# Kernel optimization log

Hardware: AMD Instinct MI355X
Metric: run time of the kernel (lower is better)

The kernel has to match this reference:

```python
import jax, jax.numpy as jnp
import numpy as np

N = 100000
E = 1600000
H = 64      # hidden_size
NH = 8      # num_heads
DH = H // NH  # per-head dim (heads are the LAST axis, as in the torch code)


def _lin(x, W, b):
    return x @ W + b


def setup_inputs() -> dict:
    key = jax.random.key(0)
    ks = jax.random.split(key, 18)
    s = 0.05
    inp = {
        "h_x": jax.random.normal(ks[0], (N, H), jnp.float32),
        "h_e": jax.random.normal(ks[1], (E, H), jnp.float32),
        "row": jax.random.randint(ks[2], (E,), 0, N, jnp.int32),  # dst node of each nonzero
        "col": jax.random.randint(ks[3], (E,), 0, N, jnp.int32),  # src node of each nonzero
    }
    names = ["q", "k", "v", "e", "oh", "oe"]
    for i, nm in enumerate(names):
        inp["W" + nm] = jax.random.normal(ks[4 + 2 * i], (H, H), jnp.float32) * s
        inp["b" + nm] = jax.random.normal(ks[5 + 2 * i], (H,), jnp.float32) * s
    return inp


def reference(h_x, h_e, row, col, Wq, bq, Wk, bk, Wv, bv, We, be, Woh, boh, Woe, boe):
    n = h_x.shape[0]
    m = h_e.shape[0]
    q = _lin(h_x, Wq, bq).reshape(n, DH, NH)
    k = _lin(h_x, Wk, bk).reshape(n, DH, NH)
    v = _lin(h_x, Wv, bv).reshape(n, DH, NH)
    e = _lin(h_e, We, be).reshape(m, DH, NH)

    # SDDMM: per-nonzero (i=row, j=col), per-head dot of q[i] and k[j]  -> (E, NH)
    scores = (q[row] * k[col]).sum(axis=1) / jnp.sqrt(jnp.float32(DH))

    # edge gating: e.sum over dh axis -> (E, NH)
    e_gate = e.sum(axis=1)
    scores = scores * e_gate

    # oe branch (uses pre-softmax gated scores)
    oe_feat = scores[:, None, :] * e          # (E, DH, NH)
    oe = _lin(oe_feat.reshape(m, H), Woe, boe)

    # sparse softmax over dim=1 (per destination row), per head
    mx = jax.ops.segment_max(scores, row, num_segments=n)      # (N, NH)
    ex = jnp.exp(scores - mx[row])
    den = jax.ops.segment_sum(ex, row, num_segments=n)         # (N, NH)
    sm = ex / den[row]                                          # (E, NH)

    # bSpMM: h_out[i,:,h] = sum_{e: row[e]=i} sm[e,h] * v[col[e],:,h]
    h_out = jax.ops.segment_sum(sm[:, None, :] * v[col], row, num_segments=n)
    oh = _lin(h_out.reshape(n, H), Woh, boh)
    return (oh, oe)
```

## Files before the change

kernel.cpp:

```cpp
#include <hip/hip_runtime.h>

typedef __attribute__((ext_vector_type(8))) short bf16x8;
typedef __attribute__((ext_vector_type(4))) float f32x4;

__device__ __forceinline__ unsigned short f2bf(float f) {
  unsigned u = __float_as_uint(f);
  return (unsigned short)((u + 0x7fffu + ((u >> 16) & 1u)) >> 16);
}
__device__ __forceinline__ float bf2f(unsigned short h) {
  return __uint_as_float(((unsigned)h) << 16);
}

__device__ __forceinline__ void lds_fence() {
  asm volatile("s_waitcnt lgkmcnt(0)" ::: "memory");
  __builtin_amdgcn_sched_barrier(0);
}

template<bool IN_BF16, bool OUT_BF16>
__global__ void __launch_bounds__(256) gemm64_kernel(const void* __restrict__ Ain,
    const float* __restrict__ W, const float* __restrict__ bias,
    void* __restrict__ Out, int M) {
  const int tid = threadIdx.x;
  const int l = tid & 63;
  const int g = l >> 4;
  const int n15 = l & 15;

  bf16x8 bfrag[4][2];
  float bv[4];
#pragma unroll
  for (int nb = 0; nb < 4; ++nb) {
    bv[nb] = bias[nb * 16 + n15];
#pragma unroll
    for (int kb = 0; kb < 2; ++kb)
#pragma unroll
      for (int j = 0; j < 8; ++j)
        bfrag[nb][kb][j] = (short)f2bf(W[(kb * 32 + g * 8 + j) * 64 + nb * 16 + n15]);
  }

  int wid = (blockIdx.x * blockDim.x + tid) >> 6;
  int nw = (gridDim.x * blockDim.x) >> 6;
  int ntiles = (M + 15) >> 4;
  for (int t = wid; t < ntiles; t += nw) {
    int m0 = t << 4;
    int arow = m0 + n15;
    bf16x8 a0, a1;
    if (arow < M) {
      if constexpr (IN_BF16) {
        const unsigned short* ap = (const unsigned short*)Ain + (size_t)arow * 64 + g * 8;
        a0 = *(const bf16x8*)ap;
        a1 = *(const bf16x8*)(ap + 32);
      } else {
        const float* ap = (const float*)Ain + (size_t)arow * 64 + g * 8;
        f32x4 x0 = *(const f32x4*)ap, x1 = *(const f32x4*)(ap + 4);
        f32x4 x2 = *(const f32x4*)(ap + 32), x3 = *(const f32x4*)(ap + 36);
#pragma unroll
        for (int j = 0; j < 4; ++j) {
          a0[j] = (short)f2bf(x0[j]); a0[4 + j] = (short)f2bf(x1[j]);
          a1[j] = (short)f2bf(x2[j]); a1[4 + j] = (short)f2bf(x3[j]);
        }
      }
    } else {
#pragma unroll
      for (int j = 0; j < 8; ++j) { a0[j] = 0; a1[j] = 0; }
    }
    f32x4 acc[4];
#pragma unroll
    for (int nb = 0; nb < 4; ++nb) {
      acc[nb] = (f32x4){bv[nb], bv[nb], bv[nb], bv[nb]};
      acc[nb] = __builtin_amdgcn_mfma_f32_16x16x32_bf16(a0, bfrag[nb][0], acc[nb], 0, 0, 0);
      acc[nb] = __builtin_amdgcn_mfma_f32_16x16x32_bf16(a1, bfrag[nb][1], acc[nb], 0, 0, 0);
    }
#pragma unroll
    for (int nb = 0; nb < 4; ++nb)
#pragma unroll
      for (int r = 0; r < 4; ++r) {
        int orow = m0 + g * 4 + r;
        if (orow < M) {
          float val = acc[nb][r];
          size_t oidx = (size_t)orow * 64 + nb * 16 + n15;
          if constexpr (OUT_BF16) ((unsigned short*)Out)[oidx] = f2bf(val);
          else                    ((float*)Out)[oidx] = val;
        }
      }
  }
}

__global__ void __launch_bounds__(256) qkv3_kernel(const float* __restrict__ hx,
    const float* __restrict__ Wq, const float* __restrict__ bq,
    const float* __restrict__ Wk, const float* __restrict__ bk,
    const float* __restrict__ Wv, const float* __restrict__ bv,
    unsigned short* __restrict__ q, unsigned short* __restrict__ k,
    unsigned short* __restrict__ v, int M) {
  const int tid = threadIdx.x;
  const int l = tid & 63;
  const int g = l >> 4;
  const int n15 = l & 15;
  const float* Ws[3] = {Wq, Wk, Wv};
  const float* bs[3] = {bq, bk, bv};
  unsigned short* outs[3] = {q, k, v};

  bf16x8 bfrag[3][4][2];
  float bvv[3][4];
#pragma unroll
  for (int w = 0; w < 3; ++w)
#pragma unroll
    for (int nb = 0; nb < 4; ++nb) {
      bvv[w][nb] = bs[w][nb * 16 + n15];
#pragma unroll
      for (int kb = 0; kb < 2; ++kb)
#pragma unroll
        for (int j = 0; j < 8; ++j)
          bfrag[w][nb][kb][j] = (short)f2bf(Ws[w][(kb * 32 + g * 8 + j) * 64 + nb * 16 + n15]);
    }

  int wid = (blockIdx.x * blockDim.x + tid) >> 6;
  int nw = (gridDim.x * blockDim.x) >> 6;
  int ntiles = (M + 15) >> 4;
  for (int t = wid; t < ntiles; t += nw) {
    int m0 = t << 4;
    int arow = m0 + n15;
    bf16x8 a0, a1;
    if (arow < M) {
      const float* ap = hx + (size_t)arow * 64 + g * 8;
      f32x4 x0 = *(const f32x4*)ap, x1 = *(const f32x4*)(ap + 4);
      f32x4 x2 = *(const f32x4*)(ap + 32), x3 = *(const f32x4*)(ap + 36);
#pragma unroll
      for (int j = 0; j < 4; ++j) {
        a0[j] = (short)f2bf(x0[j]); a0[4 + j] = (short)f2bf(x1[j]);
        a1[j] = (short)f2bf(x2[j]); a1[4 + j] = (short)f2bf(x3[j]);
      }
    } else {
#pragma unroll
      for (int j = 0; j < 8; ++j) { a0[j] = 0; a1[j] = 0; }
    }
#pragma unroll
    for (int w = 0; w < 3; ++w) {
      f32x4 acc[4];
#pragma unroll
      for (int nb = 0; nb < 4; ++nb) {
        acc[nb] = (f32x4){bvv[w][nb], bvv[w][nb], bvv[w][nb], bvv[w][nb]};
        acc[nb] = __builtin_amdgcn_mfma_f32_16x16x32_bf16(a0, bfrag[w][nb][0], acc[nb], 0, 0, 0);
        acc[nb] = __builtin_amdgcn_mfma_f32_16x16x32_bf16(a1, bfrag[w][nb][1], acc[nb], 0, 0, 0);
      }
#pragma unroll
      for (int nb = 0; nb < 4; ++nb)
#pragma unroll
        for (int r = 0; r < 4; ++r) {
          int orow = m0 + g * 4 + r;
          if (orow < M)
            outs[w][(size_t)orow * 64 + nb * 16 + n15] = f2bf(acc[nb][r]);
        }
    }
  }
}

__global__ void __launch_bounds__(256) edge_fused_kernel(
    const float* __restrict__ he,
    const int* __restrict__ rowi, const int* __restrict__ coli,
    const int* __restrict__ eslot,
    const unsigned short* __restrict__ qb, const unsigned short* __restrict__ kbuf,
    const float* __restrict__ We, const float* __restrict__ be,
    const float* __restrict__ Woe, const float* __restrict__ boe,
    float* __restrict__ oe, float* __restrict__ escores, int E) {
  const int tid = threadIdx.x;
  const int wv = tid >> 6;
  const int l = tid & 63;
  const int g = l >> 4;
  const int n15 = l & 15;
  const int h = n15 & 7;

  __shared__ float s_lds[4][160];
  __shared__ unsigned short feat_lds[4][16 * 72];

  bf16x8 bfE[4][2], bfO[4][2];
  float beV[4], boV[4];
#pragma unroll
  for (int nb = 0; nb < 4; ++nb) {
    beV[nb] = be[nb * 16 + n15];
    boV[nb] = boe[nb * 16 + n15];
#pragma unroll
    for (int kb = 0; kb < 2; ++kb)
#pragma unroll
      for (int j = 0; j < 8; ++j) {
        bfE[nb][kb][j] = (short)f2bf(We[(kb * 32 + g * 8 + j) * 64 + nb * 16 + n15]);
        bfO[nb][kb][j] = (short)f2bf(Woe[(kb * 32 + g * 8 + j) * 64 + nb * 16 + n15]);
      }
  }

  const int ntiles = (E + 15) >> 4;
  const int nit = (ntiles + 3) >> 2;
  for (int it = blockIdx.x; it < nit; it += gridDim.x) {
    const int m0 = ((it << 2) + wv) << 4;
    const int arow = m0 + n15;
    bf16x8 a0, a1;
    if (arow < E) {
      const float* ap = he + (size_t)arow * 64 + g * 8;
      f32x4 x0 = *(const f32x4*)ap, x1 = *(const f32x4*)(ap + 4);
      f32x4 x2 = *(const f32x4*)(ap + 32), x3 = *(const f32x4*)(ap + 36);
#pragma unroll
      for (int j = 0; j < 4; ++j) {
        a0[j] = (short)f2bf(x0[j]); a0[4 + j] = (short)f2bf(x1[j]);
        a1[j] = (short)f2bf(x2[j]); a1[4 + j] = (short)f2bf(x3[j]);
      }
    } else {
#pragma unroll
      for (int j = 0; j < 8; ++j) { a0[j] = 0; a1[j] = 0; }
    }
    f32x4 acc[4];
#pragma unroll
    for (int nb = 0; nb < 4; ++nb) {
      acc[nb] = (f32x4){beV[nb], beV[nb], beV[nb], beV[nb]};
      acc[nb] = __builtin_amdgcn_mfma_f32_16x16x32_bf16(a0, bfE[nb][0], acc[nb], 0, 0, 0);
      acc[nb] = __builtin_amdgcn_mfma_f32_16x16x32_bf16(a1, bfE[nb][1], acc[nb], 0, 0, 0);
    }
    float gc[4];
#pragma unroll
    for (int r = 0; r < 4; ++r) {
      float s = acc[0][r] + acc[1][r] + acc[2][r] + acc[3][r];
      s += __shfl_xor(s, 8, 64);
      gc[r] = s * 0.35355339059327373f;
    }
    const int esafe = (arow < E) ? arow : (E - 1);
    const int rq = rowi[esafe], rc = coli[esafe];
    const int slotv = eslot[esafe];
    const unsigned short* qp = qb + (size_t)rq * 64 + g * 16;
    const unsigned short* kp = kbuf + (size_t)rc * 64 + g * 16;
    bf16x8 qv0 = *(const bf16x8*)qp, qv1 = *(const bf16x8*)(qp + 8);
    bf16x8 kv0 = *(const bf16x8*)kp, kv1 = *(const bf16x8*)(kp + 8);
    float p[8];
#pragma unroll
    for (int j = 0; j < 8; ++j)
      p[j] = bf2f((unsigned short)qv0[j]) * bf2f((unsigned short)kv0[j])
           + bf2f((unsigned short)qv1[j]) * bf2f((unsigned short)kv1[j]);
#pragma unroll
    for (int j = 0; j < 8; ++j) {
      p[j] += __shfl_xor(p[j], 16, 64);
      p[j] += __shfl_xor(p[j], 32, 64);
    }
    if (l < 16) {
      float2* sp = (float2*)&s_lds[wv][n15 * 10];
#pragma unroll
      for (int j = 0; j < 4; ++j) sp[j] = make_float2(p[2 * j], p[2 * j + 1]);
    }
    lds_fence();
    float srow[4];
#pragma unroll
    for (int r = 0; r < 4; ++r)
      srow[r] = s_lds[wv][(g * 4 + r) * 10 + h] * gc[r];
#pragma unroll
    for (int r = 0; r < 4; ++r) {
      int orow = m0 + g * 4 + r;
      int slot = __shfl(slotv, g * 4 + r, 64);
      if (n15 < 8 && orow < E) escores[(size_t)slot * 8 + n15] = srow[r];
    }
#pragma unroll
    for (int nb = 0; nb < 4; ++nb)
#pragma unroll
      for (int r = 0; r < 4; ++r)
        feat_lds[wv][(g * 4 + r) * 72 + nb * 16 + n15] = f2bf(srow[r] * acc[nb][r]);
    lds_fence();
    const unsigned short* fpt = &feat_lds[wv][n15 * 72 + g * 8];
    a0 = *(const bf16x8*)fpt;
    a1 = *(const bf16x8*)(fpt + 32);
#pragma unroll
    for (int nb = 0; nb < 4; ++nb) {
      f32x4 a2 = (f32x4){boV[nb], boV[nb], boV[nb], boV[nb]};
      a2 = __builtin_amdgcn_mfma_f32_16x16x32_bf16(a0, bfO[nb][0], a2, 0, 0, 0);
      a2 = __builtin_amdgcn_mfma_f32_16x16x32_bf16(a1, bfO[nb][1], a2, 0, 0, 0);
#pragma unroll
      for (int r = 0; r < 4; ++r) {
        int orow = m0 + g * 4 + r;
        if (orow < E) oe[(size_t)orow * 64 + nb * 16 + n15] = a2[r];
      }
    }
  }
}

__global__ void zero_kernel(int* __restrict__ p, int n) {
  int i = blockIdx.x * blockDim.x + threadIdx.x;
  if (i < n) p[i] = 0;
}

__global__ void hist_kernel(const int* __restrict__ row, int* __restrict__ deg, int E) {
  int gid = blockIdx.x * blockDim.x + threadIdx.x;
  if (gid < E) atomicAdd(&deg[row[gid]], 1);
}

#define SCAN_B 256
#define SCAN_E 8
__global__ void scan1_kernel(const int* __restrict__ deg, int* __restrict__ rowptr,
                             int* __restrict__ blksum, int n) {
  __shared__ int sh[SCAN_B];
  int base = blockIdx.x * (SCAN_B * SCAN_E) + threadIdx.x * SCAN_E;
  int v[SCAN_E];
  int s = 0;
#pragma unroll
  for (int j = 0; j < SCAN_E; ++j) {
    v[j] = (base + j < n) ? deg[base + j] : 0;
    s += v[j];
  }
  sh[threadIdx.x] = s;
  __syncthreads();
  for (int off = 1; off < SCAN_B; off <<= 1) {
    int t = (threadIdx.x >= off) ? sh[threadIdx.x - off] : 0;
    __syncthreads();
    sh[threadIdx.x] += t;
    __syncthreads();
  }
  if (threadIdx.x == SCAN_B - 1) blksum[blockIdx.x] = sh[SCAN_B - 1];
  int run = sh[threadIdx.x] - s;
#pragma unroll
  for (int j = 0; j < SCAN_E; ++j) {
    if (base + j < n) rowptr[base + j] = run;
    run += v[j];
  }
}

__global__ void scan2_kernel(int* __restrict__ blksum, int nb) {
  __shared__ int sh[SCAN_B];
  int v = (threadIdx.x < nb) ? blksum[threadIdx.x] : 0;
  sh[threadIdx.x] = v;
  __syncthreads();
  for (int off = 1; off < SCAN_B; off <<= 1) {
    int t = (threadIdx.x >= off) ? sh[threadIdx.x - off] : 0;
    __syncthreads();
    sh[threadIdx.x] += t;
    __syncthreads();
  }
  if (threadIdx.x < nb) blksum[threadIdx.x] = sh[threadIdx.x] - v;
}

__global__ void scan3_kernel(int* __restrict__ rowptr, int* __restrict__ cursor,
                             const int* __restrict__ blksum, int n) {
  int i = blockIdx.x * blockDim.x + threadIdx.x;
  if (i >= n) return;
  int v = rowptr[i] + blksum[i / (SCAN_B * SCAN_E)];
  rowptr[i] = v;
  cursor[i] = v;
}

__global__ void scatter_kernel(const int* __restrict__ row, const int* __restrict__ col,
                               int* __restrict__ cursor, int* __restrict__ eslot,
                               int* __restrict__ ecol, int E) {
  int gid = blockIdx.x * blockDim.x + threadIdx.x;
  if (gid >= E) return;
  int r = row[gid];
  int slot = atomicAdd(&cursor[r], 1);
  eslot[gid] = slot;
  ecol[slot] = col[gid];
}

__global__ void __launch_bounds__(256) row_attn_kernel(const float* __restrict__ escores,
    const int* __restrict__ rowptr, const int* __restrict__ deg,
    const int* __restrict__ ecol,
    const unsigned short* __restrict__ vb, float* __restrict__ hout, int n) {
  int gid = blockIdx.x * blockDim.x + threadIdx.x;
  int r = gid >> 6, lane = threadIdx.x & 63;
  if (r >= n) return;
  int start = rowptr[r], dg = deg[r];
  int h = lane & 7;
  float den = 0.f, acc = 0.f;
#pragma unroll 4
  for (int i = 0; i < dg; ++i) {
    int c = ecol[start + i];
    float ex = __expf(escores[(size_t)(start + i) * 8 + h]);
    float vv = bf2f(vb[(size_t)c * 64 + lane]);
    den += ex;
    acc += ex * vv;
  }
  hout[(size_t)r * 64 + lane] = (dg > 0) ? acc / den : 0.f;
}

extern "C" void kernel_launch(void* const* d_in, const int* in_sizes, int n_in,
                              void* d_out, int out_size, void* d_ws, size_t ws_size,
                              hipStream_t stream) {
  const float* hx  = (const float*)d_in[0];
  const float* he  = (const float*)d_in[1];
  const int*   row = (const int*)d_in[2];
  const int*   col = (const int*)d_in[3];
  const float* Wq = (const float*)d_in[4],  *bq = (const float*)d_in[5];
  const float* Wk = (const float*)d_in[6],  *bk = (const float*)d_in[7];
  const float* Wv = (const float*)d_in[8],  *bv = (const float*)d_in[9];
  const float* We = (const float*)d_in[10], *be = (const float*)d_in[11];
  const float* Woh = (const float*)d_in[12], *boh = (const float*)d_in[13];
  const float* Woe = (const float*)d_in[14], *boe = (const float*)d_in[15];

  const int n = in_sizes[0] / 64;
  const int E = in_sizes[2];

  float* out = (float*)d_out;
  float* oh = out;
  float* oe = out + (size_t)n * 64;

  unsigned short* qb   = (unsigned short*)d_ws;
  unsigned short* kb   = qb + (size_t)n * 64;
  unsigned short* vbuf = kb + (size_t)n * 64;
  float* escores = (float*)(vbuf + (size_t)n * 64);
  float* hout    = escores + (size_t)E * 8;

  int* deg    = (int*)(hout + (size_t)n * 64);
  int* rowptr = deg + n;
  int* cursor = rowptr + n;
  int* blksum = cursor + n;
  int* eslot  = blksum + 256;
  int* ecol   = eslot + (size_t)E;

  const int nb_scan = (n + SCAN_B * SCAN_E - 1) / (SCAN_B * SCAN_E);

  zero_kernel<<<(n + 255) / 256, 256, 0, stream>>>(deg, n);
  hist_kernel<<<(E + 255) / 256, 256, 0, stream>>>(row, deg, E);
  scan1_kernel<<<nb_scan, SCAN_B, 0, stream>>>(deg, rowptr, blksum, n);
  scan2_kernel<<<1, SCAN_B, 0, stream>>>(blksum, nb_scan);
  scan3_kernel<<<(n + 255) / 256, 256, 0, stream>>>(rowptr, cursor, blksum, n);
  scatter_kernel<<<(E + 255) / 256, 256, 0, stream>>>(row, col, cursor, eslot, ecol, E);

  qkv3_kernel<<<512, 256, 0, stream>>>(hx, Wq, bq, Wk, bk, Wv, bv, qb, kb, vbuf, n);
  edge_fused_kernel<<<2048, 256, 0, stream>>>(he, row, col, eslot, qb, kb, We, be,
                                              Woe, boe, oe, escores, E);

  row_attn_kernel<<<(n + 3) / 4, 256, 0, stream>>>(escores, rowptr, deg, ecol,
                                                   vbuf, hout, n);
  gemm64_kernel<false, false><<<512, 256, 0, stream>>>(hout, Woh, boh, oh, n);
}
```

Measured before the change: 568.0 us.

## Prefetch next edge tile and use hardware packed bf16 conversion

```diff
diff --git a/kernel.cpp b/kernel.cpp
--- a/kernel.cpp
+++ b/kernel.cpp
@@ -3,17 +3,24 @@
 typedef __attribute__((ext_vector_type(8))) short bf16x8;
 typedef __attribute__((ext_vector_type(4))) float f32x4;
 
-__device__ __forceinline__ unsigned short f2bf(float f) {
-  unsigned u = __float_as_uint(f);
-  return (unsigned short)((u + 0x7fffu + ((u >> 16) & 1u)) >> 16);
-}
 __device__ __forceinline__ float bf2f(unsigned short h) {
   return __uint_as_float(((unsigned)h) << 16);
 }
-
-__device__ __forceinline__ void lds_fence() {
-  asm volatile("s_waitcnt lgkmcnt(0)" ::: "memory");
-  __builtin_amdgcn_sched_barrier(0);
+__device__ __forceinline__ unsigned cvtpk(float a, float b) {
+  unsigned r;
+  asm("v_cvt_pk_bf16_f32 %0, %1, %2" : "=v"(r) : "v"(a), "v"(b));
+  return r;
+}
+__device__ __forceinline__ unsigned short f2bf(float f) {
+  return (unsigned short)(cvtpk(f, f) & 0xffffu);
+}
+__device__ __forceinline__ bf16x8 pack8(f32x4 x0, f32x4 x1) {
+  union { bf16x8 v; unsigned u[4]; } z;
+  z.u[0] = cvtpk(x0[0], x0[1]);
+  z.u[1] = cvtpk(x0[2], x0[3]);
+  z.u[2] = cvtpk(x1[0], x1[1]);
+  z.u[3] = cvtpk(x1[2], x1[3]);
+  return z.v;
 }
 
 template<bool IN_BF16, bool OUT_BF16>
@@ -51,13 +58,8 @@
         a1 = *(const bf16x8*)(ap + 32);
       } else {
         const float* ap = (const float*)Ain + (size_t)arow * 64 + g * 8;
-        f32x4 x0 = *(const f32x4*)ap, x1 = *(const f32x4*)(ap + 4);
-        f32x4 x2 = *(const f32x4*)(ap + 32), x3 = *(const f32x4*)(ap + 36);
-#pragma unroll
-        for (int j = 0; j < 4; ++j) {
-          a0[j] = (short)f2bf(x0[j]); a0[4 + j] = (short)f2bf(x1[j]);
-          a1[j] = (short)f2bf(x2[j]); a1[4 + j] = (short)f2bf(x3[j]);
-        }
+        a0 = pack8(*(const f32x4*)ap, *(const f32x4*)(ap + 4));
+        a1 = pack8(*(const f32x4*)(ap + 32), *(const f32x4*)(ap + 36));
       }
     } else {
 #pragma unroll
@@ -122,13 +124,8 @@
     bf16x8 a0, a1;
     if (arow < M) {
       const float* ap = hx + (size_t)arow * 64 + g * 8;
-      f32x4 x0 = *(const f32x4*)ap, x1 = *(const f32x4*)(ap + 4);
-      f32x4 x2 = *(const f32x4*)(ap + 32), x3 = *(const f32x4*)(ap + 36);
-#pragma unroll
-      for (int j = 0; j < 4; ++j) {
-        a0[j] = (short)f2bf(x0[j]); a0[4 + j] = (short)f2bf(x1[j]);
-        a1[j] = (short)f2bf(x2[j]); a1[4 + j] = (short)f2bf(x3[j]);
-      }
+      a0 = pack8(*(const f32x4*)ap, *(const f32x4*)(ap + 4));
+      a1 = pack8(*(const f32x4*)(ap + 32), *(const f32x4*)(ap + 36));
     } else {
 #pragma unroll
       for (int j = 0; j < 8; ++j) { a0[j] = 0; a1[j] = 0; }
@@ -154,7 +151,7 @@
   }
 }
 
-__global__ void __launch_bounds__(256) edge_fused_kernel(
+__global__ void __launch_bounds__(256, 4) edge_fused_kernel(
     const float* __restrict__ he,
     const int* __restrict__ rowi, const int* __restrict__ coli,
     const int* __restrict__ eslot,
@@ -189,20 +186,46 @@
 
   const int ntiles = (E + 15) >> 4;
   const int nit = (ntiles + 3) >> 2;
-  for (int it = blockIdx.x; it < nit; it += gridDim.x) {
+  const int stride = gridDim.x;
+
+  int it = blockIdx.x;
+  if (it >= nit) return;
+
+  f32x4 h0, h1, h2, h3;
+  int rq, rc, sl;
+  {
+    int m0 = ((it << 2) + wv) << 4;
+    int es = min(m0 + n15, E - 1);
+    const float* ap = he + (size_t)es * 64 + g * 8;
+    h0 = *(const f32x4*)ap;       h1 = *(const f32x4*)(ap + 4);
+    h2 = *(const f32x4*)(ap + 32); h3 = *(const f32x4*)(ap + 36);
+    rq = rowi[es]; rc = coli[es]; sl = eslot[es];
+  }
+
+  while (true) {
     const int m0 = ((it << 2) + wv) << 4;
     const int arow = m0 + n15;
-    bf16x8 a0, a1;
-    if (arow < E) {
-      const float* ap = he + (size_t)arow * 64 + g * 8;
-      f32x4 x0 = *(const f32x4*)ap, x1 = *(const f32x4*)(ap + 4);
-      f32x4 x2 = *(const f32x4*)(ap + 32), x3 = *(const f32x4*)(ap + 36);
-#pragma unroll
-      for (int j = 0; j < 4; ++j) {
-        a0[j] = (short)f2bf(x0[j]); a0[4 + j] = (short)f2bf(x1[j]);
-        a1[j] = (short)f2bf(x2[j]); a1[4 + j] = (short)f2bf(x3[j]);
-      }
-    } else {
+
+    const unsigned short* qp = qb + (size_t)rq * 64 + g * 16;
+    const unsigned short* kp = kbuf + (size_t)rc * 64 + g * 16;
+    bf16x8 qv0 = *(const bf16x8*)qp, qv1 = *(const bf16x8*)(qp + 8);
+    bf16x8 kv0 = *(const bf16x8*)kp, kv1 = *(const bf16x8*)(kp + 8);
+
+    const int itn = it + stride;
+    const bool more = itn < nit;
+    f32x4 nh0 = h0, nh1 = h1, nh2 = h2, nh3 = h3;
+    int nrq = rq, nrc = rc, nsl = sl;
+    if (more) {
+      int m0n = ((itn << 2) + wv) << 4;
+      int es = min(m0n + n15, E - 1);
+      const float* ap = he + (size_t)es * 64 + g * 8;
+      nh0 = *(const f32x4*)ap;       nh1 = *(const f32x4*)(ap + 4);
+      nh2 = *(const f32x4*)(ap + 32); nh3 = *(const f32x4*)(ap + 36);
+      nrq = rowi[es]; nrc = coli[es]; nsl = eslot[es];
+    }
+
+    bf16x8 a0 = pack8(h0, h1), a1 = pack8(h2, h3);
+    if (arow >= E) {
 #pragma unroll
       for (int j = 0; j < 8; ++j) { a0[j] = 0; a1[j] = 0; }
     }
@@ -220,13 +243,6 @@
       s += __shfl_xor(s, 8, 64);
       gc[r] = s * 0.35355339059327373f;
     }
-    const int esafe = (arow < E) ? arow : (E - 1);
-    const int rq = rowi[esafe], rc = coli[esafe];
-    const int slotv = eslot[esafe];
-    const unsigned short* qp = qb + (size_t)rq * 64 + g * 16;
-    const unsigned short* kp = kbuf + (size_t)rc * 64 + g * 16;
-    bf16x8 qv0 = *(const bf16x8*)qp, qv1 = *(const bf16x8*)(qp + 8);
-    bf16x8 kv0 = *(const bf16x8*)kp, kv1 = *(const bf16x8*)(kp + 8);
     float p[8];
 #pragma unroll
     for (int j = 0; j < 8; ++j)
@@ -242,7 +258,6 @@
 #pragma unroll
       for (int j = 0; j < 4; ++j) sp[j] = make_float2(p[2 * j], p[2 * j + 1]);
     }
-    lds_fence();
     float srow[4];
 #pragma unroll
     for (int r = 0; r < 4; ++r)
@@ -250,7 +265,7 @@
 #pragma unroll
     for (int r = 0; r < 4; ++r) {
       int orow = m0 + g * 4 + r;
-      int slot = __shfl(slotv, g * 4 + r, 64);
+      int slot = __shfl(sl, g * 4 + r, 64);
       if (n15 < 8 && orow < E) escores[(size_t)slot * 8 + n15] = srow[r];
     }
 #pragma unroll
@@ -258,7 +273,6 @@
 #pragma unroll
       for (int r = 0; r < 4; ++r)
         feat_lds[wv][(g * 4 + r) * 72 + nb * 16 + n15] = f2bf(srow[r] * acc[nb][r]);
-    lds_fence();
     const unsigned short* fpt = &feat_lds[wv][n15 * 72 + g * 8];
     a0 = *(const bf16x8*)fpt;
     a1 = *(const bf16x8*)(fpt + 32);
@@ -273,6 +287,11 @@
         if (orow < E) oe[(size_t)orow * 64 + nb * 16 + n15] = a2[r];
       }
     }
+
+    if (!more) break;
+    h0 = nh0; h1 = nh1; h2 = nh2; h3 = nh3;
+    rq = nrq; rc = nrc; sl = nsl;
+    it = itn;
   }
 }
 
```

After: 757.5 us. 33.4% more time.
